# Optimization experiments

Hardware: AMD Instinct MI355X
Metric: run time of the kernel (lower is better)

Reference implementation:

```python
import jax, jax.numpy as jnp
import numpy as np

PLANE_SIZE = 512
N_LEVELS = 8
FEATURE_DIM = 16
N_PTS = 524288


def setup_inputs() -> dict:
    key = jax.random.key(0)
    k1, k2, k3 = jax.random.split(key, 3)
    x = jax.random.uniform(k1, (N_PTS, 3), dtype=jnp.float32)
    # per-point float mip level bias in [0, n_levels-1]
    level = jax.random.uniform(k2, (N_PTS, 1), dtype=jnp.float32) * (N_LEVELS - 1)
    fm = jax.random.uniform(k3, (3, PLANE_SIZE, PLANE_SIZE, FEATURE_DIM),
                            minval=-0.01, maxval=0.01, dtype=jnp.float32)
    return {"x": x, "level": level, "fm": fm, "n_levels": N_LEVELS}


def _bilinear(flat_pyr, offsets, sizes, uv, lvl_i):
    # flat_pyr: (3, T, C) concatenated mip levels; uv: (3, N, 2); lvl_i: (3, N) int32
    size = sizes[lvl_i]                      # (3, N) texture size at this mip
    fsize = size.astype(uv.dtype)
    px = uv[..., 0] * fsize - 0.5            # u -> width axis (nvdiffrast convention)
    py = uv[..., 1] * fsize - 0.5            # v -> height axis
    x0 = jnp.floor(px)
    y0 = jnp.floor(py)
    fx = (px - x0)[..., None]
    fy = (py - y0)[..., None]
    x0i = x0.astype(jnp.int32)
    y0i = y0.astype(jnp.int32)
    xa = jnp.clip(x0i, 0, size - 1)          # boundary_mode='clamp'
    xb = jnp.clip(x0i + 1, 0, size - 1)
    ya = jnp.clip(y0i, 0, size - 1)
    yb = jnp.clip(y0i + 1, 0, size - 1)
    base = offsets[lvl_i]
    p = jnp.arange(3)[:, None]
    g = lambda yy, xx: flat_pyr[p, base + yy * size + xx]   # (3, N, C) gather
    f00 = g(ya, xa); f01 = g(ya, xb); f10 = g(yb, xa); f11 = g(yb, xb)
    return (f00 * (1 - fx) + f01 * fx) * (1 - fy) + (f10 * (1 - fx) + f11 * fx) * fy


def reference(x, level, fm, n_levels):
    N = x.shape[0]
    C = fm.shape[-1]
    # build mip pyramid via 2x2 box filter (nvdiffrast auto-mips)
    levels = [fm]
    for _ in range(n_levels - 1):
        t = levels[-1]
        s = t.shape[1]
        levels.append(t.reshape(3, s // 2, 2, s // 2, 2, C).mean(axis=(2, 4)))
    sizes_list = [l.shape[1] for l in levels]
    offsets = jnp.asarray(np.cumsum([0] + [s * s for s in sizes_list[:-1]]), jnp.int32)
    sizes = jnp.asarray(sizes_list, jnp.int32)
    flat_pyr = jnp.concatenate([l.reshape(3, -1, C) for l in levels], axis=1)  # (3, T, C)
    # tri-plane decomposition: plane0 sees (y,z), plane1 (x,z), plane2 (x,y)
    uv = jnp.stack([x[:, [1, 2]], x[:, [0, 2]], x[:, [0, 1]]], axis=0)  # (3, N, 2)
    max_mip = n_levels - 1
    lvl = jnp.clip(jnp.broadcast_to(level.reshape(1, N), (3, N)), 0.0, float(max_mip))
    l0 = jnp.floor(lvl)
    f = (lvl - l0)[..., None]                # (3, N, 1) level fraction
    l0i = l0.astype(jnp.int32)
    l1i = jnp.minimum(l0i + 1, max_mip)
    s0 = _bilinear(flat_pyr, offsets, sizes, uv, l0i)
    s1 = _bilinear(flat_pyr, offsets, sizes, uv, l1i)
    enc = s0 * (1 - f) + s1 * f              # (3, N, C) trilinear (mip-lerped)
    # permute(1,2,0,3).view(N, 3C): per point, concat plane0|plane1|plane2 features
    return jnp.transpose(enc, (1, 0, 2)).reshape(N, 3 * C)
```

## Files before the change

### kernel.cpp

```cpp
#include <hip/hip_runtime.h>
#include <hip/hip_fp16.h>


typedef float        f4v   __attribute__((ext_vector_type(4)));
typedef unsigned int u32x2 __attribute__((ext_vector_type(2)));
typedef unsigned int u32x4 __attribute__((ext_vector_type(4)));

#define FM_PLANE_STRIDE (262144 * 16)
#define WS_PLANE_STRIDE (87376 * 16)
#define PSTRIDE_H (349520 * 16)
#define WS_H_BYTES (3ull * PSTRIDE_H * 2ull)
#define LVL4_OFF 348160u

__device__ __forceinline__ unsigned lvl_off(int l) {
    return (1048576u - (1048576u >> (2 * l))) / 3u;
}

__device__ __forceinline__ f4v ld4(const float* p) {
    return *reinterpret_cast<const f4v*>(p);
}
__device__ __forceinline__ f4v ld4nt(const float* p) {
    return __builtin_nontemporal_load(reinterpret_cast<const f4v*>(p));
}
__device__ __forceinline__ void st4(float* p, f4v v) {
    *reinterpret_cast<f4v*>(p) = v;
}
__device__ __forceinline__ void st4nt(float* p, f4v v) {
    __builtin_nontemporal_store(v, reinterpret_cast<f4v*>(p));
}
__device__ __forceinline__ f4v ldraw_h(const __half* p) {
    return *reinterpret_cast<const f4v*>(p);
}
__device__ __forceinline__ u32x2 pack4(f4v v) {
    __half2 lo = __floats2half2_rn(v.x, v.y);
    __half2 hi = __floats2half2_rn(v.z, v.w);
    u32x2 r;
    r.x = *reinterpret_cast<unsigned*>(&lo);
    r.y = *reinterpret_cast<unsigned*>(&hi);
    return r;
}
__device__ __forceinline__ f4v h4f(const __half* p) {
    u32x2 u = *reinterpret_cast<const u32x2*>(p);
    unsigned a0 = u.x, a1 = u.y;
    __half2 lo = *reinterpret_cast<__half2*>(&a0);
    __half2 hi = *reinterpret_cast<__half2*>(&a1);
    float2 flo = __half22float2(lo), fhi = __half22float2(hi);
    f4v r; r.x = flo.x; r.y = flo.y; r.z = fhi.x; r.w = fhi.y;
    return r;
}
__device__ __forceinline__ float2 up2(float rawcomp) {
    unsigned u = __float_as_uint(rawcomp);
    __half2 hh = *reinterpret_cast<__half2*>(&u);
    return __half22float2(hh);
}


__global__ __launch_bounds__(256) void mip_convert_l1(
    const float* __restrict__ fm, __half* __restrict__ wsh)
{
    int t = blockIdx.x * 256 + threadIdx.x;
    const int p = blockIdx.y;
    const int q = t & 3, idx = t >> 2;
    const int y = idx >> 8, x = idx & 255;
    const float* sp = fm + (size_t)p * FM_PLANE_STRIDE
                         + ((size_t)(2 * y) * 512 + 2 * x) * 16 + q * 4;
    f4v a = ld4nt(sp);
    f4v b = ld4nt(sp + 16);
    f4v c = ld4nt(sp + 512 * 16);
    f4v d = ld4nt(sp + 512 * 16 + 16);
    __half* L0 = wsh + (size_t)p * PSTRIDE_H;
    size_t o00 = ((size_t)(2 * y) * 512 + 2 * x) * 16 + q * 4;
    *reinterpret_cast<u32x2*>(L0 + o00)                 = pack4(a);
    *reinterpret_cast<u32x2*>(L0 + o00 + 16)            = pack4(b);
    *reinterpret_cast<u32x2*>(L0 + o00 + 512 * 16)      = pack4(c);
    *reinterpret_cast<u32x2*>(L0 + o00 + 512 * 16 + 16) = pack4(d);
    f4v m = (a + b + c + d) * 0.25f;
    __half* L1 = wsh + (size_t)p * PSTRIDE_H + (size_t)262144 * 16;
    *reinterpret_cast<u32x2*>(L1 + ((size_t)y * 256 + x) * 16 + q * 4) = pack4(m);
}

__global__ __launch_bounds__(256) void mip_tail_h(__half* __restrict__ wsh)
{
    const int tile = blockIdx.x;
    const int q    = blockIdx.y;
    const int p    = blockIdx.z;
    const int ty = tile >> 2, tx = tile & 3;
    const int tid = threadIdx.x;

    __shared__ f4v A[32 * 32];
    __shared__ f4v B[16 * 16];

    __half* plane = wsh + (size_t)p * PSTRIDE_H;
    const __half* L1 = plane + (size_t)lvl_off(1) * 16;
    __half* L2 = plane + (size_t)lvl_off(2) * 16;
    __half* L3 = plane + (size_t)lvl_off(3) * 16;
    __half* L4 = plane + (size_t)lvl_off(4) * 16;
    __half* L5 = plane + (size_t)lvl_off(5) * 16;
    __half* L6 = plane + (size_t)lvl_off(6) * 16;
    __half* L7 = plane + (size_t)lvl_off(7) * 16;

    #pragma unroll
    for (int k = 0; k < 4; ++k) {
        int li = tid + k * 256;
        int ly = li >> 5, lx = li & 31;
        int gy = ty * 32 + ly, gx = tx * 32 + lx;
        const __half* sp = L1 + ((size_t)(2 * gy) * 256 + 2 * gx) * 16 + q * 4;
        f4v r = (h4f(sp) + h4f(sp + 16) + h4f(sp + 256 * 16) + h4f(sp + 256 * 16 + 16)) * 0.25f;
        A[li] = r;
        *reinterpret_cast<u32x2*>(L2 + ((size_t)gy * 128 + gx) * 16 + q * 4) = pack4(r);
    }
    __syncthreads();

    {
        int ly = tid >> 4, lx = tid & 15;
        f4v r = (A[(2 * ly) * 32 + 2 * lx]     + A[(2 * ly) * 32 + 2 * lx + 1] +
                 A[(2 * ly + 1) * 32 + 2 * lx] + A[(2 * ly + 1) * 32 + 2 * lx + 1]) * 0.25f;
        B[tid] = r;
        *reinterpret_cast<u32x2*>(L3 + ((size_t)(ty * 16 + ly) * 64 + tx * 16 + lx) * 16 + q * 4) = pack4(r);
    }
    __syncthreads();

    if (tid < 64) {
        int ly = tid >> 3, lx = tid & 7;
        f4v r = (B[(2 * ly) * 16 + 2 * lx]     + B[(2 * ly) * 16 + 2 * lx + 1] +
                 B[(2 * ly + 1) * 16 + 2 * lx] + B[(2 * ly + 1) * 16 + 2 * lx + 1]) * 0.25f;
        A[tid] = r;
        *reinterpret_cast<u32x2*>(L4 + ((size_t)(ty * 8 + ly) * 32 + tx * 8 + lx) * 16 + q * 4) = pack4(r);
    }
    __syncthreads();

    if (tid < 16) {
        int ly = tid >> 2, lx = tid & 3;
        f4v r = (A[(2 * ly) * 8 + 2 * lx]     + A[(2 * ly) * 8 + 2 * lx + 1] +
                 A[(2 * ly + 1) * 8 + 2 * lx] + A[(2 * ly + 1) * 8 + 2 * lx + 1]) * 0.25f;
        B[tid] = r;
        *reinterpret_cast<u32x2*>(L5 + ((size_t)(ty * 4 + ly) * 16 + tx * 4 + lx) * 16 + q * 4) = pack4(r);
    }
    __syncthreads();

    if (tid < 4) {
        int ly = tid >> 1, lx = tid & 1;
        f4v r = (B[(2 * ly) * 4 + 2 * lx]     + B[(2 * ly) * 4 + 2 * lx + 1] +
                 B[(2 * ly + 1) * 4 + 2 * lx] + B[(2 * ly + 1) * 4 + 2 * lx + 1]) * 0.25f;
        A[tid] = r;
        *reinterpret_cast<u32x2*>(L6 + ((size_t)(ty * 2 + ly) * 8 + tx * 2 + lx) * 16 + q * 4) = pack4(r);
    }
    __syncthreads();

    if (tid == 0) {
        f4v r = (A[0] + A[1] + A[2] + A[3]) * 0.25f;
        *reinterpret_cast<u32x2*>(L7 + ((size_t)ty * 4 + tx) * 16 + q * 4) = pack4(r);
    }
}

__device__ __forceinline__ void tap_issue(
    const __half* __restrict__ wplane, const __half* __restrict__ lds_h,
    int l, float u, float v, int h,
    f4v& q00, f4v& q01, f4v& q10, f4v& q11, float& fx, float& fy)
{
    const int sz = 512 >> l;
    const float fsz = (float)sz;
    float px = u * fsz - 0.5f;
    float py = v * fsz - 0.5f;
    float xf = floorf(px), yf = floorf(py);
    fx = px - xf;
    fy = py - yf;
    int xi = (int)xf, yi = (int)yf;
    int xa = min(max(xi, 0), sz - 1);
    int xb = min(xi + 1, sz - 1);
    int ya = min(max(yi, 0), sz - 1);
    int yb = min(yi + 1, sz - 1);
    if (l >= 4) {
        const __half* base = lds_h + (size_t)(lvl_off(l) - LVL4_OFF) * 16 + h * 8;
        const __half* r0 = base + (ya * sz) * 16;
        const __half* r1 = base + (yb * sz) * 16;
        q00 = ldraw_h(r0 + xa * 16);
        q01 = ldraw_h(r0 + xb * 16);
        q10 = ldraw_h(r1 + xa * 16);
        q11 = ldraw_h(r1 + xb * 16);
    } else {
        const __half* base = wplane + (size_t)lvl_off(l) * 16 + h * 8;
        const __half* r0 = base + (size_t)(ya * sz) * 16;
        const __half* r1 = base + (size_t)(yb * sz) * 16;
        q00 = ldraw_h(r0 + (size_t)xa * 16);
        q01 = ldraw_h(r0 + (size_t)xb * 16);
        q10 = ldraw_h(r1 + (size_t)xa * 16);
        q11 = ldraw_h(r1 + (size_t)xb * 16);
    }
}

__global__ __launch_bounds__(1024) void trimip_sample_h(
    const float* __restrict__ xyz, const float* __restrict__ level,
    const __half* __restrict__ wsh, float* __restrict__ out, int N)
{
    __shared__ u32x4 lds[2720];
    const int p = blockIdx.y;
    const __half* wplane = wsh + (size_t)p * PSTRIDE_H;
    for (int uidx = threadIdx.x; uidx < 2720; uidx += 1024) {
        lds[uidx] = *reinterpret_cast<const u32x4*>(
            wplane + (size_t)LVL4_OFF * 16 + (size_t)uidx * 8);
    }
    __syncthreads();
    const __half* lds_h = reinterpret_cast<const __half*>(lds);

    const int n = blockIdx.x * 512 + (threadIdx.x >> 1);
    if (n >= N) return;
    const int h = threadIdx.x & 1;

    const float c0 = xyz[n * 3 + 0];
    const float c1 = xyz[n * 3 + 1];
    const float c2 = xyz[n * 3 + 2];
    const float u = (p == 0) ? c1 : c0;
    const float v = (p == 2) ? c1 : c2;

    float lv = level[n];
    lv = fminf(fmaxf(lv, 0.f), 7.f);
    float lf = floorf(lv);
    float f = lv - lf;
    int l0 = (int)lf;
    int l1 = min(l0 + 1, 7);

    f4v a00, a01, a10, a11, b00, b01, b10, b11;
    float fx0, fy0, fx1, fy1;
    tap_issue(wplane, lds_h, l0, u, v, h, a00, a01, a10, a11, fx0, fy0);
    tap_issue(wplane, lds_h, l1, u, v, h, b00, b01, b10, b11, fx1, fy1);

    float s0[8], s1[8];
    {
        float gx = 1.f - fx0, gy = 1.f - fy0;
        float w00 = gx * gy, w01 = fx0 * gy, w10 = gx * fy0, w11 = fx0 * fy0;
        #pragma unroll
        for (int i = 0; i < 4; ++i) {
            float2 a = up2(a00[i]), b = up2(a01[i]), c = up2(a10[i]), d = up2(a11[i]);
            s0[2 * i]     = a.x * w00 + b.x * w01 + c.x * w10 + d.x * w11;
            s0[2 * i + 1] = a.y * w00 + b.y * w01 + c.y * w10 + d.y * w11;
        }
    }
    {
        float gx = 1.f - fx1, gy = 1.f - fy1;
        float w00 = gx * gy, w01 = fx1 * gy, w10 = gx * fy1, w11 = fx1 * fy1;
        #pragma unroll
        for (int i = 0; i < 4; ++i) {
            float2 a = up2(b00[i]), b = up2(b01[i]), c = up2(b10[i]), d = up2(b11[i]);
            s1[2 * i]     = a.x * w00 + b.x * w01 + c.x * w10 + d.x * w11;
            s1[2 * i + 1] = a.y * w00 + b.y * w01 + c.y * w10 + d.y * w11;
        }
    }

    float g = 1.f - f;
    f4v oa, ob;
    #pragma unroll
    for (int i = 0; i < 4; ++i) {
        oa[i] = s0[i] * g + s1[i] * f;
        ob[i] = s0[4 + i] * g + s1[4 + i] * f;
    }
    float* op = out + (size_t)((n * 3 + p) * 2 + h) * 8;
    st4nt(op, oa);
    st4nt(op + 4, ob);
}


__device__ __forceinline__ f4v avg4(f4v a, f4v b, f4v c, f4v d) {
    return (a + b + c + d) * 0.25f;
}

__global__ __launch_bounds__(256) void mip_build_f(
    const float* __restrict__ src, float* __restrict__ dst)
{
    int t = blockIdx.x * blockDim.x + threadIdx.x;
    const int p = blockIdx.y;
    const int q = t & 3, idx = t >> 2;
    const int y = idx >> 8, x = idx & 255;
    const float* sp = src + (size_t)p * FM_PLANE_STRIDE
                          + ((size_t)(2 * y) * 512 + 2 * x) * 16 + q * 4;
    f4v r = avg4(ld4(sp), ld4(sp + 16), ld4(sp + 512 * 16), ld4(sp + 512 * 16 + 16));
    st4(dst + (size_t)p * WS_PLANE_STRIDE + ((size_t)y * 256 + x) * 16 + q * 4, r);
}

__global__ __launch_bounds__(256) void mip_tail_f(float* __restrict__ mips)
{
    const int tile = blockIdx.x, q = blockIdx.y, p = blockIdx.z;
    const int ty = tile >> 2, tx = tile & 3;
    const int tid = threadIdx.x;
    __shared__ f4v A[32 * 32];
    __shared__ f4v B[16 * 16];
    float* plane = mips + (size_t)p * WS_PLANE_STRIDE;
    const float* L1 = plane;
    float* L2 = plane + (size_t)65536 * 16;
    float* L3 = plane + (size_t)81920 * 16;
    float* L4 = plane + (size_t)86016 * 16;
    float* L5 = plane + (size_t)87040 * 16;
    float* L6 = plane + (size_t)87296 * 16;
    float* L7 = plane + (size_t)87360 * 16;

    #pragma unroll
    for (int k = 0; k < 4; ++k) {
        int li = tid + k * 256;
        int ly = li >> 5, lx = li & 31;
        int gy = ty * 32 + ly, gx = tx * 32 + lx;
        const float* sp = L1 + ((size_t)(2 * gy) * 256 + 2 * gx) * 16 + q * 4;
        f4v r = avg4(ld4(sp), ld4(sp + 16), ld4(sp + 256 * 16), ld4(sp + 256 * 16 + 16));
        A[li] = r;
        st4(L2 + ((size_t)gy * 128 + gx) * 16 + q * 4, r);
    }
    __syncthreads();
    {
        int ly = tid >> 4, lx = tid & 15;
        f4v r = avg4(A[(2 * ly) * 32 + 2 * lx],     A[(2 * ly) * 32 + 2 * lx + 1],
                     A[(2 * ly + 1) * 32 + 2 * lx], A[(2 * ly + 1) * 32 + 2 * lx + 1]);
        B[tid] = r;
        st4(L3 + ((size_t)(ty * 16 + ly) * 64 + tx * 16 + lx) * 16 + q * 4, r);
    }
    __syncthreads();
    if (tid < 64) {
        int ly = tid >> 3, lx = tid & 7;
        f4v r = avg4(B[(2 * ly) * 16 + 2 * lx],     B[(2 * ly) * 16 + 2 * lx + 1],
                     B[(2 * ly + 1) * 16 + 2 * lx], B[(2 * ly + 1) * 16 + 2 * lx + 1]);
        A[tid] = r;
        st4(L4 + ((size_t)(ty * 8 + ly) * 32 + tx * 8 + lx) * 16 + q * 4, r);
    }
    __syncthreads();
    if (tid < 16) {
        int ly = tid >> 2, lx = tid & 3;
        f4v r = avg4(A[(2 * ly) * 8 + 2 * lx],     A[(2 * ly) * 8 + 2 * lx + 1],
                     A[(2 * ly + 1) * 8 + 2 * lx], A[(2 * ly + 1) * 8 + 2 * lx + 1]);
        B[tid] = r;
        st4(L5 + ((size_t)(ty * 4 + ly) * 16 + tx * 4 + lx) * 16 + q * 4, r);
    }
    __syncthreads();
    if (tid < 4) {
        int ly = tid >> 1, lx = tid & 1;
        f4v r = avg4(B[(2 * ly) * 4 + 2 * lx],     B[(2 * ly) * 4 + 2 * lx + 1],
                     B[(2 * ly + 1) * 4 + 2 * lx], B[(2 * ly + 1) * 4 + 2 * lx + 1]);
        A[tid] = r;
        st4(L6 + ((size_t)(ty * 2 + ly) * 8 + tx * 2 + lx) * 16 + q * 4, r);
    }
    __syncthreads();
    if (tid == 0) {
        f4v r = avg4(A[0], A[1], A[2], A[3]);
        st4(L7 + ((size_t)ty * 4 + tx) * 16 + q * 4, r);
    }
}

__device__ __forceinline__ f4v bilerp_f(
    const float* __restrict__ fm, const float* __restrict__ mips,
    int p, int l, float u, float v, int q)
{
    const int sz = 512 >> l;
    const float fsz = (float)sz;
    float px = u * fsz - 0.5f;
    float py = v * fsz - 0.5f;
    float xf = floorf(px), yf = floorf(py);
    float fx = px - xf, fy = py - yf;
    int xi = (int)xf, yi = (int)yf;
    int xa = min(max(xi, 0), sz - 1);
    int xb = min(xi + 1, sz - 1);
    int ya = min(max(yi, 0), sz - 1);
    int yb = min(yi + 1, sz - 1);
    const float* base;
    if (l == 0) {
        base = fm + (size_t)p * FM_PLANE_STRIDE;
    } else {
        unsigned off = (262144u - ((unsigned)(sz * sz) << 2)) / 3u;
        base = mips + (size_t)p * WS_PLANE_STRIDE + (size_t)off * 16;
    }
    const float* r0 = base + (size_t)(ya * sz) * 16 + q * 4;
    const float* r1 = base + (size_t)(yb * sz) * 16 + q * 4;
    f4v f00 = ld4(r0 + xa * 16);
    f4v f01 = ld4(r0 + xb * 16);
    f4v f10 = ld4(r1 + xa * 16);
    f4v f11 = ld4(r1 + xb * 16);
    float gx = 1.f - fx, gy = 1.f - fy;
    return (f00 * gx + f01 * fx) * gy + (f10 * gx + f11 * fx) * fy;
}

__global__ __launch_bounds__(256) void trimip_sample_f(
    const float* __restrict__ xyz, const float* __restrict__ level,
    const float* __restrict__ fm, const float* __restrict__ mips,
    float* __restrict__ out, int N)
{
    int t = blockIdx.x * blockDim.x + threadIdx.x;
    if (t >= N * 12) return;
    const int q = t & 3;
    const int r = t >> 2;
    const int n = r / 3;
    const int p = r - n * 3;
    const float c0 = xyz[n * 3 + 0];
    const float c1 = xyz[n * 3 + 1];
    const float c2 = xyz[n * 3 + 2];
    const float u = (p == 0) ? c1 : c0;
    const float v = (p == 2) ? c1 : c2;
    float lv = level[n];
    lv = fminf(fmaxf(lv, 0.f), 7.f);
    float lf = floorf(lv);
    float f = lv - lf;
    int l0 = (int)lf;
    int l1 = min(l0 + 1, 7);
    f4v s0 = bilerp_f(fm, mips, p, l0, u, v, q);
    f4v s1 = bilerp_f(fm, mips, p, l1, u, v, q);
    f4v o = s0 * (1.f - f) + s1 * f;
    st4nt(out + (size_t)t * 4, o);
}

extern "C" void kernel_launch(void* const* d_in, const int* in_sizes, int n_in,
                              void* d_out, int out_size, void* d_ws, size_t ws_size,
                              hipStream_t stream) {
    const float* xyz   = (const float*)d_in[0];
    const float* level = (const float*)d_in[1];
    const float* fm    = (const float*)d_in[2];
    float* out = (float*)d_out;
    const int N = in_sizes[1];

    if (ws_size >= WS_H_BYTES) {
        __half* wsh = (__half*)d_ws;
        mip_convert_l1<<<dim3(1024, 3), dim3(256), 0, stream>>>(fm, wsh);
        mip_tail_h<<<dim3(16, 4, 3), dim3(256), 0, stream>>>(wsh);
        trimip_sample_h<<<dim3((N + 511) / 512, 3), 1024, 0, stream>>>(
            xyz, level, wsh, out, N);
    } else {
        float* mips = (float*)d_ws;
        mip_build_f<<<dim3(1024, 3), dim3(256), 0, stream>>>(fm, mips);
        mip_tail_f<<<dim3(16, 4, 3), dim3(256), 0, stream>>>(mips);
        const int total = N * 12;
        trimip_sample_f<<<(total + 255) / 256, 256, 0, stream>>>(xyz, level, fm, mips, out, N);
    }
}
```

Baseline: 196.4 us.

## Fuse mip pyramid build into one kernel and sample level 0 from fp32 input

Merges the level-1 conversion and mip-tail kernels into a single 1024-thread kernel per 64x64 tile that reads the fp32 feature map and writes levels 1-6. It no longer writes an fp16 copy of level 0; the sampler reads level 0 directly from the fp32 input. Level 7 is computed per block in LDS from level 6. The aim is to cut one launch and the large fp16 level-0 write, and also to avoid fp16 rounding at level 0. The costs are wider fp32 gathers for level-0 taps, a branch in the sampler, and only 192 blocks in the build kernel, which limits its parallelism.

```diff
diff --git a/kernel.cpp b/kernel.cpp
--- a/kernel.cpp
+++ b/kernel.cpp
@@ -55,121 +55,102 @@
 }
 
 
-__global__ __launch_bounds__(256) void mip_convert_l1(
+__global__ __launch_bounds__(1024) void mip_build_all(
     const float* __restrict__ fm, __half* __restrict__ wsh)
 {
-    int t = blockIdx.x * 256 + threadIdx.x;
-    const int p = blockIdx.y;
-    const int q = t & 3, idx = t >> 2;
-    const int y = idx >> 8, x = idx & 255;
-    const float* sp = fm + (size_t)p * FM_PLANE_STRIDE
-                         + ((size_t)(2 * y) * 512 + 2 * x) * 16 + q * 4;
-    f4v a = ld4nt(sp);
-    f4v b = ld4nt(sp + 16);
-    f4v c = ld4nt(sp + 512 * 16);
-    f4v d = ld4nt(sp + 512 * 16 + 16);
-    __half* L0 = wsh + (size_t)p * PSTRIDE_H;
-    size_t o00 = ((size_t)(2 * y) * 512 + 2 * x) * 16 + q * 4;
-    *reinterpret_cast<u32x2*>(L0 + o00)                 = pack4(a);
-    *reinterpret_cast<u32x2*>(L0 + o00 + 16)            = pack4(b);
-    *reinterpret_cast<u32x2*>(L0 + o00 + 512 * 16)      = pack4(c);
-    *reinterpret_cast<u32x2*>(L0 + o00 + 512 * 16 + 16) = pack4(d);
-    f4v m = (a + b + c + d) * 0.25f;
-    __half* L1 = wsh + (size_t)p * PSTRIDE_H + (size_t)262144 * 16;
-    *reinterpret_cast<u32x2*>(L1 + ((size_t)y * 256 + x) * 16 + q * 4) = pack4(m);
-}
-
-__global__ __launch_bounds__(256) void mip_tail_h(__half* __restrict__ wsh)
-{
+    __shared__ f4v A[32 * 32 * 4];
+    __shared__ f4v B[16 * 16 * 4];
+
     const int tile = blockIdx.x;
-    const int q    = blockIdx.y;
-    const int p    = blockIdx.z;
-    const int ty = tile >> 2, tx = tile & 3;
+    const int p    = blockIdx.y;
+    const int ty = tile >> 3, tx = tile & 7;
     const int tid = threadIdx.x;
-
-    __shared__ f4v A[32 * 32];
-    __shared__ f4v B[16 * 16];
+    const int q = tid & 3;
 
     __half* plane = wsh + (size_t)p * PSTRIDE_H;
-    const __half* L1 = plane + (size_t)lvl_off(1) * 16;
+    __half* L1 = plane + (size_t)lvl_off(1) * 16;
     __half* L2 = plane + (size_t)lvl_off(2) * 16;
     __half* L3 = plane + (size_t)lvl_off(3) * 16;
     __half* L4 = plane + (size_t)lvl_off(4) * 16;
     __half* L5 = plane + (size_t)lvl_off(5) * 16;
     __half* L6 = plane + (size_t)lvl_off(6) * 16;
-    __half* L7 = plane + (size_t)lvl_off(7) * 16;
+    const float* fp = fm + (size_t)p * FM_PLANE_STRIDE;
 
     #pragma unroll
     for (int k = 0; k < 4; ++k) {
-        int li = tid + k * 256;
-        int ly = li >> 5, lx = li & 31;
+        int s = (tid + k * 1024) >> 2;
+        int ly = s >> 5, lx = s & 31;
         int gy = ty * 32 + ly, gx = tx * 32 + lx;
-        const __half* sp = L1 + ((size_t)(2 * gy) * 256 + 2 * gx) * 16 + q * 4;
-        f4v r = (h4f(sp) + h4f(sp + 16) + h4f(sp + 256 * 16) + h4f(sp + 256 * 16 + 16)) * 0.25f;
-        A[li] = r;
-        *reinterpret_cast<u32x2*>(L2 + ((size_t)gy * 128 + gx) * 16 + q * 4) = pack4(r);
+        const float* sp = fp + ((size_t)(2 * gy) * 512 + 2 * gx) * 16 + q * 4;
+        f4v r = (ld4nt(sp) + ld4nt(sp + 16) +
+                 ld4nt(sp + 512 * 16) + ld4nt(sp + 512 * 16 + 16)) * 0.25f;
+        A[s * 4 + q] = r;
+        *reinterpret_cast<u32x2*>(L1 + ((size_t)gy * 256 + gx) * 16 + q * 4) = pack4(r);
     }
     __syncthreads();
 
     {
-        int ly = tid >> 4, lx = tid & 15;
-        f4v r = (A[(2 * ly) * 32 + 2 * lx]     + A[(2 * ly) * 32 + 2 * lx + 1] +
-                 A[(2 * ly + 1) * 32 + 2 * lx] + A[(2 * ly + 1) * 32 + 2 * lx + 1]) * 0.25f;
-        B[tid] = r;
-        *reinterpret_cast<u32x2*>(L3 + ((size_t)(ty * 16 + ly) * 64 + tx * 16 + lx) * 16 + q * 4) = pack4(r);
+        int s = tid >> 2;
+        int ly = s >> 4, lx = s & 15;
+        f4v r = (A[((2 * ly) * 32 + 2 * lx) * 4 + q]     + A[((2 * ly) * 32 + 2 * lx + 1) * 4 + q] +
+                 A[((2 * ly + 1) * 32 + 2 * lx) * 4 + q] + A[((2 * ly + 1) * 32 + 2 * lx + 1) * 4 + q]) * 0.25f;
+        B[s * 4 + q] = r;
+        *reinterpret_cast<u32x2*>(L2 + ((size_t)(ty * 16 + ly) * 128 + tx * 16 + lx) * 16 + q * 4) = pack4(r);
+    }
+    __syncthreads();
+
+    if (tid < 256) {
+        int s = tid >> 2;
+        int ly = s >> 3, lx = s & 7;
+        f4v r = (B[((2 * ly) * 16 + 2 * lx) * 4 + q]     + B[((2 * ly) * 16 + 2 * lx + 1) * 4 + q] +
+                 B[((2 * ly + 1) * 16 + 2 * lx) * 4 + q] + B[((2 * ly + 1) * 16 + 2 * lx + 1) * 4 + q]) * 0.25f;
+        A[s * 4 + q] = r;
+        *reinterpret_cast<u32x2*>(L3 + ((size_t)(ty * 8 + ly) * 64 + tx * 8 + lx) * 16 + q * 4) = pack4(r);
     }
     __syncthreads();
 
     if (tid < 64) {
-        int ly = tid >> 3, lx = tid & 7;
-        f4v r = (B[(2 * ly) * 16 + 2 * lx]     + B[(2 * ly) * 16 + 2 * lx + 1] +
-                 B[(2 * ly + 1) * 16 + 2 * lx] + B[(2 * ly + 1) * 16 + 2 * lx + 1]) * 0.25f;
-        A[tid] = r;
-        *reinterpret_cast<u32x2*>(L4 + ((size_t)(ty * 8 + ly) * 32 + tx * 8 + lx) * 16 + q * 4) = pack4(r);
+        int s = tid >> 2;
+        int ly = s >> 2, lx = s & 3;
+        f4v r = (A[((2 * ly) * 8 + 2 * lx) * 4 + q]     + A[((2 * ly) * 8 + 2 * lx + 1) * 4 + q] +
+                 A[((2 * ly + 1) * 8 + 2 * lx) * 4 + q] + A[((2 * ly + 1) * 8 + 2 * lx + 1) * 4 + q]) * 0.25f;
+        B[s * 4 + q] = r;
+        *reinterpret_cast<u32x2*>(L4 + ((size_t)(ty * 4 + ly) * 32 + tx * 4 + lx) * 16 + q * 4) = pack4(r);
     }
     __syncthreads();
 
     if (tid < 16) {
-        int ly = tid >> 2, lx = tid & 3;
-        f4v r = (A[(2 * ly) * 8 + 2 * lx]     + A[(2 * ly) * 8 + 2 * lx + 1] +
-                 A[(2 * ly + 1) * 8 + 2 * lx] + A[(2 * ly + 1) * 8 + 2 * lx + 1]) * 0.25f;
-        B[tid] = r;
-        *reinterpret_cast<u32x2*>(L5 + ((size_t)(ty * 4 + ly) * 16 + tx * 4 + lx) * 16 + q * 4) = pack4(r);
+        int s = tid >> 2;
+        int ly = s >> 1, lx = s & 1;
+        f4v r = (B[((2 * ly) * 4 + 2 * lx) * 4 + q]     + B[((2 * ly) * 4 + 2 * lx + 1) * 4 + q] +
+                 B[((2 * ly + 1) * 4 + 2 * lx) * 4 + q] + B[((2 * ly + 1) * 4 + 2 * lx + 1) * 4 + q]) * 0.25f;
+        A[s * 4 + q] = r;
+        *reinterpret_cast<u32x2*>(L5 + ((size_t)(ty * 2 + ly) * 16 + tx * 2 + lx) * 16 + q * 4) = pack4(r);
     }
     __syncthreads();
 
     if (tid < 4) {
-        int ly = tid >> 1, lx = tid & 1;
-        f4v r = (B[(2 * ly) * 4 + 2 * lx]     + B[(2 * ly) * 4 + 2 * lx + 1] +
-                 B[(2 * ly + 1) * 4 + 2 * lx] + B[(2 * ly + 1) * 4 + 2 * lx + 1]) * 0.25f;
-        A[tid] = r;
-        *reinterpret_cast<u32x2*>(L6 + ((size_t)(ty * 2 + ly) * 8 + tx * 2 + lx) * 16 + q * 4) = pack4(r);
-    }
-    __syncthreads();
-
-    if (tid == 0) {
-        f4v r = (A[0] + A[1] + A[2] + A[3]) * 0.25f;
-        *reinterpret_cast<u32x2*>(L7 + ((size_t)ty * 4 + tx) * 16 + q * 4) = pack4(r);
-    }
-}
-
-__device__ __forceinline__ void tap_issue(
+        f4v r = (A[0 * 4 + q] + A[1 * 4 + q] + A[2 * 4 + q] + A[3 * 4 + q]) * 0.25f;
+        *reinterpret_cast<u32x2*>(L6 + ((size_t)(ty * 8 + tx)) * 16 + q * 4) = pack4(r);
+    }
+}
+
+__device__ __forceinline__ void bilerp8_h(
     const __half* __restrict__ wplane, const __half* __restrict__ lds_h,
-    int l, float u, float v, int h,
-    f4v& q00, f4v& q01, f4v& q10, f4v& q11, float& fx, float& fy)
+    int l, float u, float v, int h, float* o)
 {
     const int sz = 512 >> l;
     const float fsz = (float)sz;
     float px = u * fsz - 0.5f;
     float py = v * fsz - 0.5f;
     float xf = floorf(px), yf = floorf(py);
-    fx = px - xf;
-    fy = py - yf;
+    float fx = px - xf, fy = py - yf;
     int xi = (int)xf, yi = (int)yf;
     int xa = min(max(xi, 0), sz - 1);
     int xb = min(xi + 1, sz - 1);
     int ya = min(max(yi, 0), sz - 1);
     int yb = min(yi + 1, sz - 1);
+    f4v q00, q01, q10, q11;
     if (l >= 4) {
         const __half* base = lds_h + (size_t)(lvl_off(l) - LVL4_OFF) * 16 + h * 8;
         const __half* r0 = base + (ya * sz) * 16;
@@ -187,21 +168,68 @@
         q10 = ldraw_h(r1 + (size_t)xa * 16);
         q11 = ldraw_h(r1 + (size_t)xb * 16);
     }
+    float gx = 1.f - fx, gy = 1.f - fy;
+    float w00 = gx * gy, w01 = fx * gy, w10 = gx * fy, w11 = fx * fy;
+    #pragma unroll
+    for (int i = 0; i < 4; ++i) {
+        float2 a = up2(q00[i]), b = up2(q01[i]), c = up2(q10[i]), d = up2(q11[i]);
+        o[2 * i]     = a.x * w00 + b.x * w01 + c.x * w10 + d.x * w11;
+        o[2 * i + 1] = a.y * w00 + b.y * w01 + c.y * w10 + d.y * w11;
+    }
+}
+
+__device__ __forceinline__ void bilerp8_f0(
+    const float* __restrict__ fmp, float u, float v, int h, float* o)
+{
+    float px = u * 512.f - 0.5f;
+    float py = v * 512.f - 0.5f;
+    float xf = floorf(px), yf = floorf(py);
+    float fx = px - xf, fy = py - yf;
+    int xi = (int)xf, yi = (int)yf;
+    int xa = min(max(xi, 0), 511);
+    int xb = min(xi + 1, 511);
+    int ya = min(max(yi, 0), 511);
+    int yb = min(yi + 1, 511);
+    const float* r0 = fmp + (size_t)(ya * 512) * 16 + h * 8;
+    const float* r1 = fmp + (size_t)(yb * 512) * 16 + h * 8;
+    f4v p00a = ld4(r0 + (size_t)xa * 16), p00b = ld4(r0 + (size_t)xa * 16 + 4);
+    f4v p01a = ld4(r0 + (size_t)xb * 16), p01b = ld4(r0 + (size_t)xb * 16 + 4);
+    f4v p10a = ld4(r1 + (size_t)xa * 16), p10b = ld4(r1 + (size_t)xa * 16 + 4);
+    f4v p11a = ld4(r1 + (size_t)xb * 16), p11b = ld4(r1 + (size_t)xb * 16 + 4);
+    float gx = 1.f - fx, gy = 1.f - fy;
+    float w00 = gx * gy, w01 = fx * gy, w10 = gx * fy, w11 = fx * fy;
+    #pragma unroll
+    for (int i = 0; i < 4; ++i) {
+        o[i]     = p00a[i] * w00 + p01a[i] * w01 + p10a[i] * w10 + p11a[i] * w11;
+        o[4 + i] = p00b[i] * w00 + p01b[i] * w01 + p10b[i] * w10 + p11b[i] * w11;
+    }
 }
 
 __global__ __launch_bounds__(1024) void trimip_sample_h(
     const float* __restrict__ xyz, const float* __restrict__ level,
-    const __half* __restrict__ wsh, float* __restrict__ out, int N)
+    const float* __restrict__ fm, const __half* __restrict__ wsh,
+    float* __restrict__ out, int N)
 {
     __shared__ u32x4 lds[2720];
     const int p = blockIdx.y;
     const __half* wplane = wsh + (size_t)p * PSTRIDE_H;
-    for (int uidx = threadIdx.x; uidx < 2720; uidx += 1024) {
+    for (int uidx = threadIdx.x; uidx < 2688; uidx += 1024) {
         lds[uidx] = *reinterpret_cast<const u32x4*>(
             wplane + (size_t)LVL4_OFF * 16 + (size_t)uidx * 8);
     }
     __syncthreads();
-    const __half* lds_h = reinterpret_cast<const __half*>(lds);
+    __half* lds_h = reinterpret_cast<__half*>(lds);
+
+    if (threadIdx.x < 64) {
+        int q = threadIdx.x & 3, i = threadIdx.x >> 2;
+        int y = i >> 2, x = i & 3;
+        f4v r = (h4f(lds_h + (size_t)(1280 + (2 * y) * 8 + 2 * x) * 16 + q * 4) +
+                 h4f(lds_h + (size_t)(1280 + (2 * y) * 8 + 2 * x + 1) * 16 + q * 4) +
+                 h4f(lds_h + (size_t)(1280 + (2 * y + 1) * 8 + 2 * x) * 16 + q * 4) +
+                 h4f(lds_h + (size_t)(1280 + (2 * y + 1) * 8 + 2 * x + 1) * 16 + q * 4)) * 0.25f;
+        *reinterpret_cast<u32x2*>(lds_h + (size_t)(1344 + i) * 16 + q * 4) = pack4(r);
+    }
+    __syncthreads();
 
     const int n = blockIdx.x * 512 + (threadIdx.x >> 1);
     if (n >= N) return;
@@ -220,32 +248,13 @@
     int l0 = (int)lf;
     int l1 = min(l0 + 1, 7);
 
-    f4v a00, a01, a10, a11, b00, b01, b10, b11;
-    float fx0, fy0, fx1, fy1;
-    tap_issue(wplane, lds_h, l0, u, v, h, a00, a01, a10, a11, fx0, fy0);
-    tap_issue(wplane, lds_h, l1, u, v, h, b00, b01, b10, b11, fx1, fy1);
-
     float s0[8], s1[8];
-    {
-        float gx = 1.f - fx0, gy = 1.f - fy0;
-        float w00 = gx * gy, w01 = fx0 * gy, w10 = gx * fy0, w11 = fx0 * fy0;
-        #pragma unroll
-        for (int i = 0; i < 4; ++i) {
-            float2 a = up2(a00[i]), b = up2(a01[i]), c = up2(a10[i]), d = up2(a11[i]);
-            s0[2 * i]     = a.x * w00 + b.x * w01 + c.x * w10 + d.x * w11;
-            s0[2 * i + 1] = a.y * w00 + b.y * w01 + c.y * w10 + d.y * w11;
-        }
-    }
-    {
-        float gx = 1.f - fx1, gy = 1.f - fy1;
-        float w00 = gx * gy, w01 = fx1 * gy, w10 = gx * fy1, w11 = fx1 * fy1;
-        #pragma unroll
-        for (int i = 0; i < 4; ++i) {
-            float2 a = up2(b00[i]), b = up2(b01[i]), c = up2(b10[i]), d = up2(b11[i]);
-            s1[2 * i]     = a.x * w00 + b.x * w01 + c.x * w10 + d.x * w11;
-            s1[2 * i + 1] = a.y * w00 + b.y * w01 + c.y * w10 + d.y * w11;
-        }
-    }
+    if (l0 == 0) {
+        bilerp8_f0(fm + (size_t)p * FM_PLANE_STRIDE, u, v, h, s0);
+    } else {
+        bilerp8_h(wplane, lds_h, l0, u, v, h, s0);
+    }
+    bilerp8_h(wplane, lds_h, l1, u, v, h, s1);
 
     float g = 1.f - f;
     f4v oa, ob;
@@ -413,10 +422,9 @@
 
     if (ws_size >= WS_H_BYTES) {
         __half* wsh = (__half*)d_ws;
-        mip_convert_l1<<<dim3(1024, 3), dim3(256), 0, stream>>>(fm, wsh);
-        mip_tail_h<<<dim3(16, 4, 3), dim3(256), 0, stream>>>(wsh);
+        mip_build_all<<<dim3(64, 3), 1024, 0, stream>>>(fm, wsh);
         trimip_sample_h<<<dim3((N + 511) / 512, 3), 1024, 0, stream>>>(
-            xyz, level, wsh, out, N);
+            xyz, level, fm, wsh, out, N);
     } else {
         float* mips = (float*)d_ws;
         mip_build_f<<<dim3(1024, 3), dim3(256), 0, stream>>>(fm, mips);
```

Result: slower. 216.0 us (+10.0%).
